# Optimization experiments

Measured on AMD Instinct MI355X. Metric: run time of the kernel, lower is better.

## Reference

```python
import jax, jax.numpy as jnp
import numpy as np

S, B, H = 2048, 2, 1024
NH = 16
HD = H // NH
EPS = 1e-5


def _ln(z, w, b):
    m = jnp.mean(z, axis=-1, keepdims=True)
    v = jnp.mean(jnp.square(z - m), axis=-1, keepdims=True)
    return (z - m) * jax.lax.rsqrt(v + EPS) * w + b


def setup_inputs() -> dict:
    key = jax.random.key(0)
    ks = jax.random.split(key, 8)
    std = 0.02
    return {
        "x": jax.random.normal(ks[0], (S, B, H), dtype=jnp.float32),
        "ln1_w": jnp.ones((H,), jnp.float32),
        "ln1_b": jnp.zeros((H,), jnp.float32),
        "w_qkv": jax.random.normal(ks[1], (3 * H, H), jnp.float32) * std,
        "b_qkv": jnp.zeros((3 * H,), jnp.float32),
        "w_proj": jax.random.normal(ks[2], (H, H), jnp.float32) * std,
        "b_proj": jnp.zeros((H,), jnp.float32),
        "ln2_w": jnp.ones((H,), jnp.float32),
        "ln2_b": jnp.zeros((H,), jnp.float32),
        "w_fc1": jax.random.normal(ks[3], (4 * H, H), jnp.float32) * std,
        "b_fc1": jnp.zeros((4 * H,), jnp.float32),
        "w_fc2": jax.random.normal(ks[4], (H, 4 * H), jnp.float32) * std,
        "b_fc2": jnp.zeros((H,), jnp.float32),
    }


def reference(x, ln1_w, ln1_b, w_qkv, b_qkv, w_proj, b_proj,
              ln2_w, ln2_b, w_fc1, b_fc1, w_fc2, b_fc2):
    s, b, h = x.shape
    # --- LayerNormLinear: LN then fused QKV projection ---
    residual = x
    qkv = _ln(x, ln1_w, ln1_b) @ w_qkv.T + b_qkv            # [S, B, 3H]
    # per-head interleaved packing: [S, B, NH, 3*HD] then split on last dim
    qkv = qkv.reshape(s, b, NH, 3 * HD).transpose(1, 2, 0, 3)  # [B, NH, S, 3HD]
    q, k, v = jnp.split(qkv, 3, axis=3)                      # each [B, NH, S, HD]
    # --- naive causal attention with full SxS scores ---
    scores = jnp.einsum("bhsd,bhtd->bhst", q, k) * (HD ** -0.5)
    causal = jnp.triu(jnp.ones((s, s), dtype=bool), k=1)
    scores = jnp.where(causal, -jnp.inf, scores)
    attn = jax.nn.softmax(scores, axis=-1)                   # [B, NH, S, S]
    out = jnp.einsum("bhst,bhtd->bhsd", attn, v)             # [B, NH, S, HD]
    out = out.transpose(0, 2, 1, 3).reshape(b, s, h).transpose(1, 0, 2)  # [S, B, H]
    out = out @ w_proj.T + b_proj
    x = residual + out
    # --- LayerNormMLP: LN -> fc1 -> gelu(tanh) -> fc2, residual ---
    residual = x
    hmid = jax.nn.gelu(_ln(x, ln2_w, ln2_b) @ w_fc1.T + b_fc1, approximate=True)
    x = residual + (hmid @ w_fc2.T + b_fc2)
    return x
```

## Files before the change

kernel.cpp:

```cpp
#include <hip/hip_runtime.h>
#include <math.h>

#define S_LEN 2048
#define B_SZ 2
#define NHEAD 16
#define HDIM 64
#define H_DIM 1024
#define M_ROWS (S_LEN * B_SZ)
#define LN_EPS 1e-5f
#define KSTR 72
#define SCL 0.18033688011112042f

typedef __attribute__((ext_vector_type(4))) float f32x4;
typedef __attribute__((ext_vector_type(8))) short short8;
typedef __attribute__((ext_vector_type(8))) unsigned short u16x8;
typedef __attribute__((ext_vector_type(4))) unsigned short u16x4;
typedef __attribute__((ext_vector_type(2))) unsigned short u16x2;

typedef __attribute__((address_space(3))) unsigned int lds_u32;
typedef const __attribute__((address_space(1))) unsigned int glb_u32;

__device__ __forceinline__ float bf2f(unsigned short u) {
    return __uint_as_float(((unsigned int)u) << 16);
}
__device__ __forceinline__ unsigned short f2bf(float f) {
    unsigned int u = __float_as_uint(f);
    return (unsigned short)((u + 0x7fffu + ((u >> 16) & 1u)) >> 16);
}

__global__ __launch_bounds__(256) void cast_all(const float* __restrict__ wqkv,
                                                const float* __restrict__ wproj,
                                                const float* __restrict__ wfc1,
                                                const float* __restrict__ wfc2,
                                                unsigned short* __restrict__ oqkv,
                                                unsigned short* __restrict__ oproj,
                                                unsigned short* __restrict__ ofc1,
                                                unsigned short* __restrict__ ofc2) {
    const int i = blockIdx.x * 256 + threadIdx.x;
    const float* src; unsigned short* dst; int off;
    if (i < 786432)       { src = wqkv;  dst = oqkv;  off = i; }
    else if (i < 1048576) { src = wproj; dst = oproj; off = i - 786432; }
    else if (i < 2097152) { src = wfc1;  dst = ofc1;  off = i - 1048576; }
    else                  { src = wfc2;  dst = ofc2;  off = i - 2097152; }
    f32x4 v = ((const f32x4*)src)[off];
    u16x4 o;
    o.x = f2bf(v.x); o.y = f2bf(v.y); o.z = f2bf(v.z); o.w = f2bf(v.w);
    ((u16x4*)dst)[off] = o;
}

__global__ __launch_bounds__(256) void ln_bf16(const float* __restrict__ x,
                                               const float* __restrict__ w,
                                               const float* __restrict__ b,
                                               unsigned short* __restrict__ y) {
    const int m = blockIdx.x;
    const int tid = threadIdx.x;
    const float* row = x + (size_t)m * H_DIM;

    float4 v = ((const float4*)row)[tid];
    float s  = v.x + v.y + v.z + v.w;
    float ss = v.x * v.x + v.y * v.y + v.z * v.z + v.w * v.w;

    __shared__ float rs[4], rss[4], stats[2];
    const int wave = tid >> 6, lane = tid & 63;
    for (int off = 32; off; off >>= 1) {
        s  += __shfl_down(s, off);
        ss += __shfl_down(ss, off);
    }
    if (lane == 0) { rs[wave] = s; rss[wave] = ss; }
    __syncthreads();
    if (tid == 0) {
        float S = rs[0] + rs[1] + rs[2] + rs[3];
        float SS = rss[0] + rss[1] + rss[2] + rss[3];
        float mean = S * (1.0f / H_DIM);
        float var = SS * (1.0f / H_DIM) - mean * mean;
        stats[0] = mean;
        stats[1] = rsqrtf(var + LN_EPS);
    }
    __syncthreads();
    const float mean = stats[0], inv = stats[1];
    float4 wv = ((const float4*)w)[tid];
    float4 bv = ((const float4*)b)[tid];
    u16x4 o;
    o.x = f2bf((v.x - mean) * inv * wv.x + bv.x);
    o.y = f2bf((v.y - mean) * inv * wv.y + bv.y);
    o.z = f2bf((v.z - mean) * inv * wv.z + bv.z);
    o.w = f2bf((v.w - mean) * inv * wv.w + bv.w);
    ((u16x4*)(y + (size_t)m * H_DIM))[tid] = o;
}

template <int EPI, bool BF_OUT, int TN>
__global__ __launch_bounds__(256) void gemm_mfma(const unsigned short* __restrict__ A,
                                                 const unsigned short* __restrict__ B,
                                                 const float* __restrict__ bias,
                                                 const float* __restrict__ resid,
                                                 void* __restrict__ Cout,
                                                 int M, int N, int K) {
    constexpr int NJ  = TN / 32;
    constexpr int ANI = 4;
    constexpr int BNI = TN / 32;
    __shared__ __attribute__((aligned(16))) unsigned short As[128 * 64];
    __shared__ __attribute__((aligned(16))) unsigned short Bs[TN * 64];

    const int tid = threadIdx.x;
    const int wid = tid >> 6;
    const int ln  = tid & 63;
    const int quad = ln >> 4;
    const int mr   = ln & 15;
    const int wm = (wid >> 1) * 64;
    const int wn = (wid & 1) * (TN / 2);

    const int mb = M >> 7;
    const int stripe = mb >> 3;
    const int xcd = blockIdx.x & 7;
    const int local = blockIdx.x >> 3;
    const int m0 = (xcd * stripe + (local % stripe)) << 7;
    const int n0 = (local / stripe) * TN;

    const int lr = ln >> 3, lc = ln & 7;
    const size_t Kb = (size_t)K * 2;
    const char* gA = (const char*)A + (size_t)(m0 + wid * 32 + lr) * Kb
                     + (size_t)((lc << 4) ^ (lr << 4));
    const int bwr = (TN == 128) ? wid * 32 : wid * 16;
    const char* gB = (const char*)B + (size_t)(n0 + bwr + lr) * Kb
                     + (size_t)((lc << 4) ^ (lr << 4));
    unsigned int* lA = (unsigned int*)As + wid * (ANI * 256);
    unsigned int* lB = (unsigned int*)Bs + wid * (BNI * 256);

    auto stage = [&](int kt) {
        const char* pa = gA + (size_t)kt * 128;
#pragma unroll
        for (int i = 0; i < ANI; i++)
            __builtin_amdgcn_global_load_lds((glb_u32*)(pa + (size_t)i * 8 * Kb),
                                             (lds_u32*)(lA + i * 256), 16, 0, 0);
        const char* pb = gB + (size_t)kt * 128;
#pragma unroll
        for (int i = 0; i < BNI; i++)
            __builtin_amdgcn_global_load_lds((glb_u32*)(pb + (size_t)i * 8 * Kb),
                                             (lds_u32*)(lB + i * 256), 16, 0, 0);
    };

    const f32x4 zero = {0.f, 0.f, 0.f, 0.f};
    f32x4 acc[4][NJ];
#pragma unroll
    for (int i = 0; i < 4; i++)
#pragma unroll
        for (int j = 0; j < NJ; j++) acc[i][j] = zero;

    const int nt = K >> 6;
    stage(0);

    const int swz = (mr & 7) << 3;
    for (int kt = 0; kt < nt; kt++) {
        __syncthreads();
#pragma unroll
        for (int h = 0; h < 2; h++) {
            short8 af[4], bf[NJ];
#pragma unroll
            for (int i = 0; i < 4; i++)
                af[i] = *(const short8*)(As + (wm + i * 16 + mr) * 64
                                            + ((h * 32 + quad * 8) ^ swz));
#pragma unroll
            for (int j = 0; j < NJ; j++)
                bf[j] = *(const short8*)(Bs + (wn + j * 16 + mr) * 64
                                            + ((h * 32 + quad * 8) ^ swz));
#pragma unroll
            for (int i = 0; i < 4; i++)
#pragma unroll
                for (int j = 0; j < NJ; j++)
                    acc[i][j] = __builtin_amdgcn_mfma_f32_16x16x32_bf16(bf[j], af[i], acc[i][j], 0, 0, 0);
        }
        if (kt + 1 < nt) {
            __syncthreads();
            stage(kt + 1);
        }
    }

    f32x4 bias4[NJ];
#pragma unroll
    for (int j = 0; j < NJ; j++)
        bias4[j] = *(const f32x4*)(bias + n0 + wn + j * 16 + quad * 4);

#pragma unroll
    for (int i = 0; i < 4; i++) {
        const int m = m0 + wm + i * 16 + mr;
#pragma unroll
        for (int j = 0; j < NJ; j++) {
            const int nb = n0 + wn + j * 16 + quad * 4;
            f32x4 v = acc[i][j] + bias4[j];
            if (EPI == 1) v += *(const f32x4*)(resid + (size_t)m * N + nb);
            if (EPI == 2) {
#pragma unroll
                for (int r = 0; r < 4; r++) {
                    const float t = v[r];
                    const float u = t + 0.044715f * t * t * t;
                    const float e = exp2f(2.3022112f * u);
                    v[r] = t - t / (e + 1.0f);
                }
            }
            if (BF_OUT) {
                u16x4 pk;
                pk.x = f2bf(v.x); pk.y = f2bf(v.y); pk.z = f2bf(v.z); pk.w = f2bf(v.w);
                *(u16x4*)((unsigned short*)Cout + (size_t)m * N + nb) = pk;
            } else {
                *(f32x4*)((float*)Cout + (size_t)m * N + nb) = v;
            }
        }
    }
}

__global__ __launch_bounds__(256) void attn_mfma(const unsigned short* __restrict__ qkv,
                                                 unsigned short* __restrict__ out) {
    __shared__ __attribute__((aligned(16))) unsigned short Ks[64 * KSTR];
    __shared__ __attribute__((aligned(16))) unsigned short Vs[64 * KSTR];
    __shared__ __attribute__((aligned(16))) unsigned short Ps[64 * KSTR];

    const int tid = threadIdx.x;
    const int wid = tid >> 6;
    const int ln  = tid & 63;
    const int quad = ln >> 4;
    const int mr   = ln & 15;

    const int id = blockIdx.x;
    const int local = id >> 3;
    const int bh = (id & 7) * 4 + (local >> 4);
    const int pa = local & 15;
    const int b  = bh >> 4;
    const int nh = bh & 15;
    const size_t chan = (size_t)nh * 192;

    const int ksr = tid >> 2, ksc = tid & 3;
    const int vt0 = (tid & 31) * 2, vd0 = (tid >> 5) * 8;

    u16x8 kp0, kp1, vp0, vp1;

#pragma unroll
    for (int half = 0; half < 2; half++) {
        const int qt = half ? (31 - pa) : pa;
        const int qb = qt * 64;

        short8 qf0, qf1;
        {
            const int qrow = qb + wid * 16 + mr;
            const unsigned short* gq = qkv + ((size_t)(qrow * 2 + b)) * 3072 + chan + quad * 8;
            qf0 = *(const short8*)gq;
            qf1 = *(const short8*)(gq + 32);
        }

        const f32x4 zero = {0.f, 0.f, 0.f, 0.f};
        f32x4 o[4];
        float ps = 0.f;
#pragma unroll
        for (int d = 0; d < 4; d++) o[d] = zero;

        {
            const unsigned short* gk = qkv + ((size_t)(ksr * 2 + b)) * 3072 + chan + 64 + ksc * 16;
            kp0 = *(const u16x8*)gk;
            kp1 = *(const u16x8*)(gk + 8);
            const unsigned short* gv = qkv + ((size_t)(vt0 * 2 + b)) * 3072 + chan + 128 + vd0;
            vp0 = *(const u16x8*)gv;
            vp1 = *(const u16x8*)(gv + 6144);
        }

        for (int kt = 0; kt <= qt; kt++) {
            __syncthreads();
            *(u16x8*)(Ks + ksr * KSTR + ksc * 16) = kp0;
            *(u16x8*)(Ks + ksr * KSTR + ksc * 16 + 8) = kp1;
#pragma unroll
            for (int j = 0; j < 8; j++) {
                u16x2 pr; pr.x = vp0[j]; pr.y = vp1[j];
                *(u16x2*)(Vs + (vd0 + j) * KSTR + vt0) = pr;
            }
            if (kt < qt) {
                const int nb = (kt + 1) * 64;
                const unsigned short* gk =
                    qkv + ((size_t)((nb + ksr) * 2 + b)) * 3072 + chan + 64 + ksc * 16;
                kp0 = *(const u16x8*)gk;
                kp1 = *(const u16x8*)(gk + 8);
                const unsigned short* gv =
                    qkv + ((size_t)((nb + vt0) * 2 + b)) * 3072 + chan + 128 + vd0;
                vp0 = *(const u16x8*)gv;
                vp1 = *(const u16x8*)(gv + 6144);
            }
            __syncthreads();

            f32x4 sacc[4];
#pragma unroll
            for (int n = 0; n < 4; n++) {
                sacc[n] = zero;
                const unsigned short* kb = Ks + (n * 16 + mr) * KSTR + quad * 8;
                short8 kfr0 = *(const short8*)kb;
                short8 kfr1 = *(const short8*)(kb + 32);
                sacc[n] = __builtin_amdgcn_mfma_f32_16x16x32_bf16(kfr0, qf0, sacc[n], 0, 0, 0);
                sacc[n] = __builtin_amdgcn_mfma_f32_16x16x32_bf16(kfr1, qf1, sacc[n], 0, 0, 0);
            }
            if (kt == qt) {
#pragma unroll
                for (int n = 0; n < 4; n++)
#pragma unroll
                    for (int r = 0; r < 4; r++)
                        if (n * 16 + quad * 4 + r > wid * 16 + mr) sacc[n][r] = -3.0e38f;
            }

            unsigned short* prow = Ps + (wid * 16 + mr) * KSTR + quad * 4;
#pragma unroll
            for (int n = 0; n < 4; n++) {
                u16x4 pk;
#pragma unroll
                for (int r = 0; r < 4; r++) {
                    const float p = exp2f(fminf(sacc[n][r] * SCL, 80.f));
                    ps += p;
                    pk[r] = (unsigned short)(__float_as_uint(p) >> 16);
                }
                *(u16x4*)(prow + n * 16) = pk;
            }

            {
                const unsigned short* pb = Ps + (wid * 16 + mr) * KSTR + quad * 8;
                short8 pa0 = *(const short8*)pb;
                short8 pa1 = *(const short8*)(pb + 32);
#pragma unroll
                for (int d = 0; d < 4; d++) {
                    const unsigned short* vb = Vs + (d * 16 + mr) * KSTR + quad * 8;
                    short8 vf0 = *(const short8*)vb;
                    short8 vf1 = *(const short8*)(vb + 32);
                    o[d] = __builtin_amdgcn_mfma_f32_16x16x32_bf16(vf0, pa0, o[d], 0, 0, 0);
                    o[d] = __builtin_amdgcn_mfma_f32_16x16x32_bf16(vf1, pa1, o[d], 0, 0, 0);
                }
            }
        }

        ps += __shfl_xor(ps, 16);
        ps += __shfl_xor(ps, 32);
        const float inv = 1.0f / ps;
        const int qrow = qb + wid * 16 + mr;
        unsigned short* po = out + ((size_t)(qrow * 2 + b)) * H_DIM + nh * HDIM;
#pragma unroll
        for (int d = 0; d < 4; d++) {
            u16x4 pk;
#pragma unroll
            for (int r = 0; r < 4; r++) pk[r] = f2bf(o[d][r] * inv);
            *(u16x4*)(po + d * 16 + quad * 4) = pk;
        }
    }
}

extern "C" void kernel_launch(void* const* d_in, const int* in_sizes, int n_in,
                              void* d_out, int out_size, void* d_ws, size_t ws_size,
                              hipStream_t stream) {
    const float* x      = (const float*)d_in[0];
    const float* ln1_w  = (const float*)d_in[1];
    const float* ln1_b  = (const float*)d_in[2];
    const float* w_qkv  = (const float*)d_in[3];
    const float* b_qkv  = (const float*)d_in[4];
    const float* w_proj = (const float*)d_in[5];
    const float* b_proj = (const float*)d_in[6];
    const float* ln2_w  = (const float*)d_in[7];
    const float* ln2_b  = (const float*)d_in[8];
    const float* w_fc1  = (const float*)d_in[9];
    const float* b_fc1  = (const float*)d_in[10];
    const float* w_fc2  = (const float*)d_in[11];
    const float* b_fc2  = (const float*)d_in[12];
    float* out = (float*)d_out;

    char* ws = (char*)d_ws;
    unsigned short* wqkv_bf  = (unsigned short*)(ws);
    unsigned short* wproj_bf = (unsigned short*)(ws + ((size_t)6 << 20));
    unsigned short* wfc1_bf  = (unsigned short*)(ws + ((size_t)8 << 20));
    unsigned short* wfc2_bf  = (unsigned short*)(ws + ((size_t)16 << 20));
    unsigned short* ln_buf   = (unsigned short*)(ws + ((size_t)24 << 20));
    unsigned short* qkv_bf   = (unsigned short*)(ws + ((size_t)32 << 20));
    unsigned short* attn_bf  = (unsigned short*)(ws + ((size_t)56 << 20));
    unsigned short* fc1_bf   = (unsigned short*)(ws + ((size_t)32 << 20));

    cast_all<<<12288, 256, 0, stream>>>(w_qkv, w_proj, w_fc1, w_fc2,
                                        wqkv_bf, wproj_bf, wfc1_bf, wfc2_bf);

    ln_bf16<<<M_ROWS, 256, 0, stream>>>(x, ln1_w, ln1_b, ln_buf);
    gemm_mfma<0, true, 128><<<768, 256, 0, stream>>>(
        ln_buf, wqkv_bf, b_qkv, nullptr, qkv_bf, M_ROWS, 3072, 1024);
    attn_mfma<<<512, 256, 0, stream>>>(qkv_bf, attn_bf);
    gemm_mfma<1, false, 64><<<512, 256, 0, stream>>>(
        attn_bf, wproj_bf, b_proj, x, out, M_ROWS, 1024, 1024);
    ln_bf16<<<M_ROWS, 256, 0, stream>>>(out, ln2_w, ln2_b, ln_buf);
    gemm_mfma<2, true, 128><<<1024, 256, 0, stream>>>(
        ln_buf, wfc1_bf, b_fc1, nullptr, fc1_bf, M_ROWS, 4096, 1024);
    gemm_mfma<1, false, 64><<<512, 256, 0, stream>>>(
        fc1_bf, wfc2_bf, b_fc2, out, out, M_ROWS, 1024, 4096);
}
```

Measured before the change: 350.4 us.

## Double-buffer LDS tiles in MFMA GEMM to overlap loads with compute

The GEMM kernel now keeps two sets of A/B shared-memory tiles. The next K-tile is loaded asynchronously straight into the spare buffer while MFMAs run on the current one, unrolled by two. This removes the old pattern where every K step waited for its global-to-LDS copy before computing. In exchange LDS use per block doubles, which may lower occupancy, and the loop assumes an even number of K tiles.

```diff
diff --git a/kernel.cpp b/kernel.cpp
--- a/kernel.cpp
+++ b/kernel.cpp
@@ -98,8 +98,10 @@
     constexpr int NJ  = TN / 32;
     constexpr int ANI = 4;
     constexpr int BNI = TN / 32;
-    __shared__ __attribute__((aligned(16))) unsigned short As[128 * 64];
-    __shared__ __attribute__((aligned(16))) unsigned short Bs[TN * 64];
+    __shared__ __attribute__((aligned(16))) unsigned short As0[128 * 64];
+    __shared__ __attribute__((aligned(16))) unsigned short Bs0[TN * 64];
+    __shared__ __attribute__((aligned(16))) unsigned short As1[128 * 64];
+    __shared__ __attribute__((aligned(16))) unsigned short Bs1[TN * 64];
 
     const int tid = threadIdx.x;
     const int wid = tid >> 6;
@@ -123,20 +125,20 @@
     const int bwr = (TN == 128) ? wid * 32 : wid * 16;
     const char* gB = (const char*)B + (size_t)(n0 + bwr + lr) * Kb
                      + (size_t)((lc << 4) ^ (lr << 4));
-    unsigned int* lA = (unsigned int*)As + wid * (ANI * 256);
-    unsigned int* lB = (unsigned int*)Bs + wid * (BNI * 256);
-
-    auto stage = [&](int kt) {
+
+    auto stage = [&](int kt, unsigned short* As_, unsigned short* Bs_) {
         const char* pa = gA + (size_t)kt * 128;
+        unsigned int* la = (unsigned int*)As_ + wid * (ANI * 256);
 #pragma unroll
         for (int i = 0; i < ANI; i++)
             __builtin_amdgcn_global_load_lds((glb_u32*)(pa + (size_t)i * 8 * Kb),
-                                             (lds_u32*)(lA + i * 256), 16, 0, 0);
+                                             (lds_u32*)(la + i * 256), 16, 0, 0);
         const char* pb = gB + (size_t)kt * 128;
+        unsigned int* lb = (unsigned int*)Bs_ + wid * (BNI * 256);
 #pragma unroll
         for (int i = 0; i < BNI; i++)
             __builtin_amdgcn_global_load_lds((glb_u32*)(pb + (size_t)i * 8 * Kb),
-                                             (lds_u32*)(lB + i * 256), 16, 0, 0);
+                                             (lds_u32*)(lb + i * 256), 16, 0, 0);
     };
 
     const f32x4 zero = {0.f, 0.f, 0.f, 0.f};
@@ -146,33 +148,37 @@
 #pragma unroll
         for (int j = 0; j < NJ; j++) acc[i][j] = zero;
 
+    const int swz = (mr & 7) << 3;
+    auto compute = [&](const unsigned short* As_, const unsigned short* Bs_) {
+#pragma unroll
+        for (int h = 0; h < 2; h++) {
+            short8 af[4], bfr[NJ];
+#pragma unroll
+            for (int i = 0; i < 4; i++)
+                af[i] = *(const short8*)(As_ + (wm + i * 16 + mr) * 64
+                                             + ((h * 32 + quad * 8) ^ swz));
+#pragma unroll
+            for (int j = 0; j < NJ; j++)
+                bfr[j] = *(const short8*)(Bs_ + (wn + j * 16 + mr) * 64
+                                              + ((h * 32 + quad * 8) ^ swz));
+#pragma unroll
+            for (int i = 0; i < 4; i++)
+#pragma unroll
+                for (int j = 0; j < NJ; j++)
+                    acc[i][j] = __builtin_amdgcn_mfma_f32_16x16x32_bf16(bfr[j], af[i], acc[i][j], 0, 0, 0);
+        }
+    };
+
     const int nt = K >> 6;
-    stage(0);
-
-    const int swz = (mr & 7) << 3;
-    for (int kt = 0; kt < nt; kt++) {
+    stage(0, As0, Bs0);
+    __syncthreads();
+    for (int kt = 0; kt < nt; kt += 2) {
+        stage(kt + 1, As1, Bs1);
+        compute(As0, Bs0);
         __syncthreads();
-#pragma unroll
-        for (int h = 0; h < 2; h++) {
-            short8 af[4], bf[NJ];
-#pragma unroll
-            for (int i = 0; i < 4; i++)
-                af[i] = *(const short8*)(As + (wm + i * 16 + mr) * 64
-                                            + ((h * 32 + quad * 8) ^ swz));
-#pragma unroll
-            for (int j = 0; j < NJ; j++)
-                bf[j] = *(const short8*)(Bs + (wn + j * 16 + mr) * 64
-                                            + ((h * 32 + quad * 8) ^ swz));
-#pragma unroll
-            for (int i = 0; i < 4; i++)
-#pragma unroll
-                for (int j = 0; j < NJ; j++)
-                    acc[i][j] = __builtin_amdgcn_mfma_f32_16x16x32_bf16(bf[j], af[i], acc[i][j], 0, 0, 0);
-        }
-        if (kt + 1 < nt) {
-            __syncthreads();
-            stage(kt + 1);
-        }
+        if (kt + 2 < nt) stage(kt + 2, As0, Bs0);
+        compute(As1, Bs1);
+        if (kt + 2 < nt) __syncthreads();
     }
 
     f32x4 bias4[NJ];
```

Result: no change. 344.5 us (-1.7%).
